# Kernel optimization log

Hardware: AMD Instinct MI355X
Metric: run time of the kernel (lower is better)

Reference implementation:

```python
import jax, jax.numpy as jnp
import numpy as np

N_EMBD = 1024
N_HEAD = 16
B, T = 2, 2048
LN_EPS = 1e-5


def _linear_params(key, d_in, d_out):
    k1, k2 = jax.random.split(key)
    bound = 1.0 / np.sqrt(d_in)
    W = jax.random.uniform(k1, (d_in, d_out), jnp.float32, -bound, bound)
    b = jax.random.uniform(k2, (d_out,), jnp.float32, -bound, bound)
    return W, b


def setup_inputs() -> dict:
    key = jax.random.key(0)
    ks = jax.random.split(key, 8)
    x = jax.random.normal(ks[0], (B, T, N_EMBD), jnp.float32)
    Wq, bq = _linear_params(ks[1], N_EMBD, N_EMBD)
    Wk, bk = _linear_params(ks[2], N_EMBD, N_EMBD)
    Wv, bv = _linear_params(ks[3], N_EMBD, N_EMBD)
    Wo, bo = _linear_params(ks[4], N_EMBD, N_EMBD)
    W1, b1 = _linear_params(ks[5], N_EMBD, 4 * N_EMBD)
    W2, b2 = _linear_params(ks[6], 4 * N_EMBD, N_EMBD)
    ln1_g = jnp.ones((N_EMBD,), jnp.float32)
    ln1_b = jnp.zeros((N_EMBD,), jnp.float32)
    ln2_g = jnp.ones((N_EMBD,), jnp.float32)
    ln2_b = jnp.zeros((N_EMBD,), jnp.float32)
    return dict(x=x, Wq=Wq, bq=bq, Wk=Wk, bk=bk, Wv=Wv, bv=bv, Wo=Wo, bo=bo,
                W1=W1, b1=b1, W2=W2, b2=b2,
                ln1_g=ln1_g, ln1_b=ln1_b, ln2_g=ln2_g, ln2_b=ln2_b)


def _layernorm(x, g, b):
    mu = jnp.mean(x, axis=-1, keepdims=True)
    var = jnp.mean(jnp.square(x - mu), axis=-1, keepdims=True)
    return (x - mu) * jax.lax.rsqrt(var + LN_EPS) * g + b


def _attention(x, Wq, bq, Wk, bk, Wv, bv, Wo, bo):
    Bsz, Tlen, C = x.shape
    hd = C // N_HEAD
    q = (x @ Wq + bq).reshape(Bsz, Tlen, N_HEAD, hd)
    k = (x @ Wk + bk).reshape(Bsz, Tlen, N_HEAD, hd)
    v = (x @ Wv + bv).reshape(Bsz, Tlen, N_HEAD, hd)
    scale = 1.0 / np.sqrt(hd)
    # NOTE: the original module's mask buffer is all ones -> masked_fill is a
    # no-op, so attention is FULL (non-causal) despite the class name.
    att = jnp.einsum('bqhd,bkhd->bhqk', q, k) * scale
    att = jax.nn.softmax(att, axis=-1)
    y = jnp.einsum('bhqk,bkhd->bqhd', att, v).reshape(Bsz, Tlen, C)
    return y @ Wo + bo


def reference(x, Wq, bq, Wk, bk, Wv, bv, Wo, bo, W1, b1, W2, b2,
              ln1_g, ln1_b, ln2_g, ln2_b):
    x = x + _attention(_layernorm(x, ln1_g, ln1_b), Wq, bq, Wk, bk, Wv, bv, Wo, bo)
    h = _layernorm(x, ln2_g, ln2_b)
    h = jax.nn.gelu(h @ W1 + b1, approximate=False) @ W2 + b2
    return x + h
```

## Files before the change

### kernel.cpp

```cpp
#include <hip/hip_runtime.h>
#include <hip/hip_bf16.h>
#include <math.h>


typedef __bf16 bf16x8 __attribute__((ext_vector_type(8)));
typedef float f32x4 __attribute__((ext_vector_type(4)));

__device__ __forceinline__ unsigned short f2bf(float f) {
  union { float f; unsigned int u; } v; v.f = f;
  unsigned int u = v.u;
  unsigned int r = (u + 0x7fffu + ((u >> 16) & 1u)) >> 16;
  return (unsigned short)r;
}

__device__ __forceinline__ unsigned int fbits(float f) {
  union { float f; unsigned int u; } v; v.f = f;
  return v.u;
}

__device__ __forceinline__ bf16x8 ld_bf16x8(const unsigned short* p) {
  union { uint4 u; bf16x8 v; } x;
  x.u = *(const uint4*)p;
  return x.v;
}

__device__ __forceinline__ void async_copy16(const void* g, void* l) {
  __builtin_amdgcn_global_load_lds(
      (const __attribute__((address_space(1))) void*)g,
      (__attribute__((address_space(3))) void*)l, 16, 0, 0);
}

__global__ __launch_bounds__(256) void transpose_cast_kernel(
    const float* __restrict__ W, unsigned short* __restrict__ Wt, int N, int K) {
  __shared__ unsigned short tile[32][33];
  const int n0 = blockIdx.x * 32, k0 = blockIdx.y * 32;
  const int t = threadIdx.x;
  const int r = t >> 3, cq = (t & 7) * 4;
  float4 v = *(const float4*)&W[(size_t)(k0 + r) * N + n0 + cq];
  tile[cq + 0][r] = f2bf(v.x);
  tile[cq + 1][r] = f2bf(v.y);
  tile[cq + 2][r] = f2bf(v.z);
  tile[cq + 3][r] = f2bf(v.w);
  __syncthreads();
  ushort4 o;
  o.x = tile[r][cq + 0];
  o.y = tile[r][cq + 1];
  o.z = tile[r][cq + 2];
  o.w = tile[r][cq + 3];
  *(ushort4*)&Wt[(size_t)(n0 + r) * K + k0 + cq] = o;
}

__global__ __launch_bounds__(256) void transpose_v_kernel(
    const unsigned short* __restrict__ V, unsigned short* __restrict__ Vt) {
  __shared__ unsigned short tile[32][36];
  const int kt = blockIdx.x * 32;
  const int d0 = blockIdx.y * 32;
  const int bh = blockIdx.z;
  const int bb = bh >> 4, h = bh & 15;
  const int t = threadIdx.x;
  const int r = t >> 3, c4 = (t & 7) * 4;
  ushort4 v = *(const ushort4*)&V[((size_t)bb * 2048 + kt + r) * 1024 + h * 64 + d0 + c4];
  tile[c4 + 0][r] = v.x;
  tile[c4 + 1][r] = v.y;
  tile[c4 + 2][r] = v.z;
  tile[c4 + 3][r] = v.w;
  __syncthreads();
  ushort4 o;
  o.x = tile[r][c4 + 0];
  o.y = tile[r][c4 + 1];
  o.z = tile[r][c4 + 2];
  o.w = tile[r][c4 + 3];
  *(ushort4*)&Vt[((size_t)bh * 64 + d0 + r) * 2048 + kt + c4] = o;
}

__global__ __launch_bounds__(256) void ln_kernel(
    const float* __restrict__ x, const float* __restrict__ g,
    const float* __restrict__ b, unsigned short* __restrict__ out) {
  const int row = blockIdx.x, t = threadIdx.x;
  const float4 v = ((const float4*)(x + (size_t)row * 1024))[t];
  float s = v.x + v.y + v.z + v.w;
  float s2 = v.x * v.x + v.y * v.y + v.z * v.z + v.w * v.w;
  for (int o = 32; o > 0; o >>= 1) {
    s += __shfl_xor(s, o, 64);
    s2 += __shfl_xor(s2, o, 64);
  }
  __shared__ float red[8];
  const int w = t >> 6;
  if ((t & 63) == 0) { red[w] = s; red[4 + w] = s2; }
  __syncthreads();
  s = red[0] + red[1] + red[2] + red[3];
  s2 = red[4] + red[5] + red[6] + red[7];
  const float mu = s * (1.f / 1024.f);
  const float var = s2 * (1.f / 1024.f) - mu * mu;
  const float rs = rsqrtf(var + 1e-5f);
  const float4 gg = ((const float4*)g)[t];
  const float4 bb = ((const float4*)b)[t];
  ushort4 o4;
  o4.x = f2bf((v.x - mu) * rs * gg.x + bb.x);
  o4.y = f2bf((v.y - mu) * rs * gg.y + bb.y);
  o4.z = f2bf((v.z - mu) * rs * gg.z + bb.z);
  o4.w = f2bf((v.w - mu) * rs * gg.w + bb.w);
  ((ushort4*)(out + (size_t)row * 1024))[t] = o4;
}

enum { MODE_QKV = 0, MODE_RES = 1, MODE_GELU = 2 };

#define QSCALE 0.18033688011112043f

template <int BM, int BN, int MODE>
__global__ __launch_bounds__(256) void gemm_kernel(
    const unsigned short* __restrict__ A, const unsigned short* __restrict__ Bt,
    const float* __restrict__ bias0, const float* __restrict__ bias1,
    const float* __restrict__ bias2, const float* __restrict__ residual,
    void* __restrict__ out0, void* __restrict__ out1, void* __restrict__ out2,
    int M, int N, int K) {
  constexpr int MI = BM / 32;
  constexpr int NI = BN / 32;
  __shared__ __align__(16) unsigned short As[2][BM * 32];
  __shared__ __align__(16) unsigned short Bs[2][BN * 32];
  const int t = threadIdx.x;
  const int m0 = blockIdx.y * BM, n0 = blockIdx.x * BN;
  const int l = t & 63, w = t >> 6;
  const int wm = (w >> 1) * (BM / 2), wn = (w & 1) * (BN / 2);
  const int lr = l & 15, lq = l >> 4;

  f32x4 acc[MI][NI];
#pragma unroll
  for (int i = 0; i < MI; i++)
#pragma unroll
    for (int j = 0; j < NI; j++) {
      f32x4 z = {0.f, 0.f, 0.f, 0.f};
      acc[i][j] = z;
    }

  for (int k0 = 0; k0 < K; k0 += 64) {
    __syncthreads();
#pragma unroll
    for (int h = 0; h < 2; h++)
#pragma unroll
      for (int s = 0; s < BM / 64; s++) {
        const int c = t + s * 256;
        const int row = c >> 2, k8 = (c & 3) * 8;
        async_copy16(&A[(size_t)(m0 + row) * K + k0 + h * 32 + k8],
                     &As[h][c * 8]);
      }
#pragma unroll
    for (int h = 0; h < 2; h++)
#pragma unroll
      for (int s = 0; s < BN / 64; s++) {
        const int c = t + s * 256;
        const int row = c >> 2, k8 = (c & 3) * 8;
        async_copy16(&Bt[(size_t)(n0 + row) * K + k0 + h * 32 + k8],
                     &Bs[h][c * 8]);
      }
    __syncthreads();
#pragma unroll
    for (int kk = 0; kk < 2; kk++) {
      bf16x8 af[MI], bf[NI];
#pragma unroll
      for (int mi = 0; mi < MI; mi++)
        af[mi] = ld_bf16x8(&As[kk][(wm + mi * 16 + lr) * 32 + lq * 8]);
#pragma unroll
      for (int ni = 0; ni < NI; ni++)
        bf[ni] = ld_bf16x8(&Bs[kk][(wn + ni * 16 + lr) * 32 + lq * 8]);
#pragma unroll
      for (int mi = 0; mi < MI; mi++)
#pragma unroll
        for (int ni = 0; ni < NI; ni++)
          acc[mi][ni] = __builtin_amdgcn_mfma_f32_16x16x32_bf16(
              af[mi], bf[ni], acc[mi][ni], 0, 0, 0);
    }
  }

#pragma unroll
  for (int mi = 0; mi < MI; mi++) {
#pragma unroll
    for (int ni = 0; ni < NI; ni++) {
#pragma unroll
      for (int i = 0; i < 4; i++) {
        const int gm = m0 + wm + mi * 16 + lq * 4 + i;
        const int gn = n0 + wn + ni * 16 + lr;
        const float v = acc[mi][ni][i];
        if (MODE == MODE_QKV) {
          const int sel = gn >> 10, cn = gn & 1023;
          const float* bb = sel == 0 ? bias0 : (sel == 1 ? bias1 : bias2);
          unsigned short* dst =
              (unsigned short*)(sel == 0 ? out0 : (sel == 1 ? out1 : out2));
          float u = v + bb[cn];
          if (sel == 0) u *= QSCALE;
          dst[(size_t)gm * 1024 + cn] = f2bf(u);
        } else if (MODE == MODE_RES) {
          ((float*)out0)[(size_t)gm * N + gn] =
              v + bias0[gn] + residual[(size_t)gm * N + gn];
        } else {
          const float u = v + bias0[gn];
          const float ge = 0.5f * u * (1.f + erff(u * 0.70710678118654752f));
          ((unsigned short*)out0)[(size_t)gm * N + gn] = f2bf(ge);
        }
      }
    }
  }
}

__global__ __launch_bounds__(256) void attn_kernel(
    const unsigned short* __restrict__ Q, const unsigned short* __restrict__ Kt,
    const unsigned short* __restrict__ Vt, unsigned short* __restrict__ O) {
  __shared__ __align__(16) unsigned short QPs[128 * 72];
  __shared__ __align__(16) unsigned short Ks[64 * 72];
  __shared__ __align__(16) unsigned short Vs[64 * 72];
  const int qt = blockIdx.x;
  const int bh = blockIdx.y;
  const int bb = bh >> 4, h = bh & 15;
  const int t = threadIdx.x, l = t & 63, w = t >> 6;
  const int lr = l & 15, lq = l >> 4;
  const size_t rowBase = (size_t)bb * 2048;
  const int col0 = h * 64;

#pragma unroll
  for (int s = 0; s < 4; s++) {
    const int c = t + s * 256;
    const int r = c >> 3, c8 = (c & 7) * 8;
    *(uint4*)&QPs[r * 72 + c8] =
        *(const uint4*)&Q[(rowBase + qt * 128 + r) * 1024 + col0 + c8];
  }
  __syncthreads();
  bf16x8 qf[2][2];
#pragma unroll
  for (int s = 0; s < 2; s++)
#pragma unroll
    for (int kk = 0; kk < 2; kk++)
      qf[s][kk] = ld_bf16x8(&QPs[(w * 32 + s * 16 + lr) * 72 + kk * 32 + lq * 8]);

  f32x4 oacc[2][4];
#pragma unroll
  for (int s = 0; s < 2; s++)
#pragma unroll
    for (int nt = 0; nt < 4; nt++) {
      f32x4 z = {0.f, 0.f, 0.f, 0.f};
      oacc[s][nt] = z;
    }
  float mi_[2] = {-1e30f, -1e30f};
  float lp[2] = {0.f, 0.f};

  for (int kt = 0; kt < 2048; kt += 64) {
    __syncthreads();
#pragma unroll
    for (int s = 0; s < 2; s++) {
      const int c = t + s * 256;
      const int r = c >> 3, c8 = (c & 7) * 8;
      *(uint4*)&Ks[r * 72 + c8] =
          *(const uint4*)&Kt[(rowBase + kt + r) * 1024 + col0 + c8];
      *(uint4*)&Vs[r * 72 + c8] =
          *(const uint4*)&Vt[((size_t)bh * 64 + r) * 2048 + kt + c8];
    }
    __syncthreads();

    f32x4 st[2][4];
#pragma unroll
    for (int s = 0; s < 2; s++)
#pragma unroll
      for (int nt = 0; nt < 4; nt++) {
        f32x4 z = {0.f, 0.f, 0.f, 0.f};
        st[s][nt] = z;
      }
#pragma unroll
    for (int nt = 0; nt < 4; nt++)
#pragma unroll
      for (int kk = 0; kk < 2; kk++) {
        bf16x8 kf = ld_bf16x8(&Ks[(nt * 16 + lr) * 72 + kk * 32 + lq * 8]);
        st[0][nt] = __builtin_amdgcn_mfma_f32_16x16x32_bf16(kf, qf[0][kk], st[0][nt], 0, 0, 0);
        st[1][nt] = __builtin_amdgcn_mfma_f32_16x16x32_bf16(kf, qf[1][kk], st[1][nt], 0, 0, 0);
      }

#pragma unroll
    for (int s = 0; s < 2; s++) {
      float mx = st[s][0][0];
#pragma unroll
      for (int nt = 0; nt < 4; nt++)
#pragma unroll
        for (int i = 0; i < 4; i++) mx = fmaxf(mx, st[s][nt][i]);
      mx = fmaxf(mx, __shfl_xor(mx, 16, 64));
      mx = fmaxf(mx, __shfl_xor(mx, 32, 64));
      const float mnew = fmaxf(mi_[s], mx);
      const float alpha = exp2f(mi_[s] - mnew);
      mi_[s] = mnew;
      float rsum = 0.f;
#pragma unroll
      for (int nt = 0; nt < 4; nt++)
#pragma unroll
        for (int i = 0; i < 4; i++) {
          const float p = exp2f(st[s][nt][i] - mnew);
          st[s][nt][i] = p;
          rsum += p;
        }
      lp[s] = lp[s] * alpha + rsum;
#pragma unroll
      for (int nt = 0; nt < 4; nt++) oacc[s][nt] *= alpha;
    }

#pragma unroll
    for (int s = 0; s < 2; s++)
#pragma unroll
      for (int nt = 0; nt < 4; nt++) {
        uint2 pk;
        pk.x = __builtin_amdgcn_perm(fbits(st[s][nt][1]), fbits(st[s][nt][0]), 0x07060302u);
        pk.y = __builtin_amdgcn_perm(fbits(st[s][nt][3]), fbits(st[s][nt][2]), 0x07060302u);
        *(uint2*)&QPs[(w * 32 + s * 16 + lr) * 72 + nt * 16 + lq * 4] = pk;
      }

#pragma unroll
    for (int kb = 0; kb < 2; kb++) {
      bf16x8 pf0 = ld_bf16x8(&QPs[(w * 32 + lr) * 72 + kb * 32 + lq * 8]);
      bf16x8 pf1 = ld_bf16x8(&QPs[(w * 32 + 16 + lr) * 72 + kb * 32 + lq * 8]);
#pragma unroll
      for (int nt = 0; nt < 4; nt++) {
        bf16x8 vf = ld_bf16x8(&Vs[(nt * 16 + lr) * 72 + kb * 32 + lq * 8]);
        oacc[0][nt] = __builtin_amdgcn_mfma_f32_16x16x32_bf16(pf0, vf, oacc[0][nt], 0, 0, 0);
        oacc[1][nt] = __builtin_amdgcn_mfma_f32_16x16x32_bf16(pf1, vf, oacc[1][nt], 0, 0, 0);
      }
    }
  }

#pragma unroll
  for (int s = 0; s < 2; s++) {
    float li = lp[s];
    li += __shfl_xor(li, 16, 64);
    li += __shfl_xor(li, 32, 64);
    const float inv = 1.f / li;
#pragma unroll
    for (int nt = 0; nt < 4; nt++)
#pragma unroll
      for (int i = 0; i < 4; i++) {
        const size_t orow = rowBase + qt * 128 + w * 32 + s * 16 + lq * 4 + i;
        const int ocol = col0 + nt * 16 + lr;
        O[orow * 1024 + ocol] = f2bf(oacc[s][nt][i] * inv);
      }
  }
}

extern "C" void kernel_launch(void* const* d_in, const int* in_sizes, int n_in,
                              void* d_out, int out_size, void* d_ws, size_t ws_size,
                              hipStream_t stream) {
  const float* x    = (const float*)d_in[0];
  const float* Wq   = (const float*)d_in[1];
  const float* bq   = (const float*)d_in[2];
  const float* Wk   = (const float*)d_in[3];
  const float* bk   = (const float*)d_in[4];
  const float* Wv   = (const float*)d_in[5];
  const float* bv   = (const float*)d_in[6];
  const float* Wo   = (const float*)d_in[7];
  const float* bo   = (const float*)d_in[8];
  const float* W1   = (const float*)d_in[9];
  const float* b1   = (const float*)d_in[10];
  const float* W2   = (const float*)d_in[11];
  const float* b2   = (const float*)d_in[12];
  const float* ln1g = (const float*)d_in[13];
  const float* ln1b = (const float*)d_in[14];
  const float* ln2g = (const float*)d_in[15];
  const float* ln2b = (const float*)d_in[16];

  char* ws = (char*)d_ws;
  const size_t MB = 1024ull * 1024ull;
  unsigned short* WqT = (unsigned short*)(ws + 0 * MB);
  unsigned short* WkT = (unsigned short*)(ws + 2 * MB);
  unsigned short* WvT = (unsigned short*)(ws + 4 * MB);
  unsigned short* WoT = (unsigned short*)(ws + 6 * MB);
  unsigned short* W1T = (unsigned short*)(ws + 8 * MB);
  unsigned short* W2T = (unsigned short*)(ws + 16 * MB);
  unsigned short* xn  = (unsigned short*)(ws + 24 * MB);
  unsigned short* Qb  = (unsigned short*)(ws + 32 * MB);
  unsigned short* Kb  = (unsigned short*)(ws + 40 * MB);
  unsigned short* Vb  = (unsigned short*)(ws + 48 * MB);
  unsigned short* Ob  = (unsigned short*)(ws + 56 * MB);
  float*          x1  = (float*)(ws + 64 * MB);
  unsigned short* h2  = (unsigned short*)(ws + 80 * MB);
  unsigned short* VtG = (unsigned short*)(ws + 24 * MB);
  unsigned short* Hb  = (unsigned short*)(ws + 24 * MB);

  const dim3 blk(256);

  transpose_cast_kernel<<<dim3(32, 32), blk, 0, stream>>>(Wq, WqT, 1024, 1024);
  transpose_cast_kernel<<<dim3(32, 32), blk, 0, stream>>>(Wk, WkT, 1024, 1024);
  transpose_cast_kernel<<<dim3(32, 32), blk, 0, stream>>>(Wv, WvT, 1024, 1024);
  transpose_cast_kernel<<<dim3(32, 32), blk, 0, stream>>>(Wo, WoT, 1024, 1024);
  transpose_cast_kernel<<<dim3(128, 32), blk, 0, stream>>>(W1, W1T, 4096, 1024);
  transpose_cast_kernel<<<dim3(32, 128), blk, 0, stream>>>(W2, W2T, 1024, 4096);

  ln_kernel<<<4096, blk, 0, stream>>>(x, ln1g, ln1b, xn);

  gemm_kernel<128, 128, MODE_QKV><<<dim3(24, 32), blk, 0, stream>>>(
      xn, WqT, bq, bk, bv, nullptr, Qb, Kb, Vb, 4096, 3072, 1024);

  transpose_v_kernel<<<dim3(64, 2, 32), blk, 0, stream>>>(Vb, VtG);

  attn_kernel<<<dim3(16, 32), blk, 0, stream>>>(Qb, Kb, VtG, Ob);

  gemm_kernel<64, 128, MODE_RES><<<dim3(8, 64), blk, 0, stream>>>(
      Ob, WoT, bo, nullptr, nullptr, x, x1, nullptr, nullptr, 4096, 1024, 1024);

  ln_kernel<<<4096, blk, 0, stream>>>(x1, ln2g, ln2b, h2);

  gemm_kernel<128, 128, MODE_GELU><<<dim3(32, 32), blk, 0, stream>>>(
      h2, W1T, b1, nullptr, nullptr, nullptr, Hb, nullptr, nullptr, 4096, 4096, 1024);

  gemm_kernel<64, 128, MODE_RES><<<dim3(8, 64), blk, 0, stream>>>(
      Hb, W2T, b2, nullptr, nullptr, x1, (float*)d_out, nullptr, nullptr, 4096, 1024, 4096);
}
```

Before: 425.5 us.

## Remap GEMM blocks per XCD and halve attention query tile to 64 rows

GEMM launches become 1D grids whose block IDs are remapped so that each of the eight XCDs (blocks assigned round-robin) handles a contiguous band of M tiles, improving L2 reuse of A rows within an XCD. The attention kernel now processes 64 query rows per block (16 per wave) instead of 128, doubling the grid to raise occupancy and parallelism on the many-CU device. The trade-off is that each block reloads the full K and V for half as many queries, doubling K/V traffic, with less MFMA work per LDS load.

```diff
diff --git a/kernel.cpp b/kernel.cpp
--- a/kernel.cpp
+++ b/kernel.cpp
@@ -119,7 +119,14 @@
   __shared__ __align__(16) unsigned short As[2][BM * 32];
   __shared__ __align__(16) unsigned short Bs[2][BN * 32];
   const int t = threadIdx.x;
-  const int m0 = blockIdx.y * BM, n0 = blockIdx.x * BN;
+
+  const int NT = N / BN, MT = M / BM;
+  const int bid = blockIdx.x;
+  const int xcd = bid & 7, local = bid >> 3;
+  const int mt = xcd * (MT >> 3) + local / NT;
+  const int nt_ = local % NT;
+  const int m0 = mt * BM, n0 = nt_ * BN;
+
   const int l = t & 63, w = t >> 6;
   const int wm = (w >> 1) * (BM / 2), wn = (w & 1) * (BN / 2);
   const int lr = l & 15, lq = l >> 4;
@@ -205,7 +212,7 @@
 __global__ __launch_bounds__(256) void attn_kernel(
     const unsigned short* __restrict__ Q, const unsigned short* __restrict__ Kt,
     const unsigned short* __restrict__ Vt, unsigned short* __restrict__ O) {
-  __shared__ __align__(16) unsigned short QPs[128 * 72];
+  __shared__ __align__(16) unsigned short QPs[64 * 72];
   __shared__ __align__(16) unsigned short Ks[64 * 72];
   __shared__ __align__(16) unsigned short Vs[64 * 72];
   const int qt = blockIdx.x;
@@ -217,30 +224,26 @@
   const int col0 = h * 64;
 
 #pragma unroll
-  for (int s = 0; s < 4; s++) {
+  for (int s = 0; s < 2; s++) {
     const int c = t + s * 256;
     const int r = c >> 3, c8 = (c & 7) * 8;
     *(uint4*)&QPs[r * 72 + c8] =
-        *(const uint4*)&Q[(rowBase + qt * 128 + r) * 1024 + col0 + c8];
+        *(const uint4*)&Q[(rowBase + qt * 64 + r) * 1024 + col0 + c8];
   }
   __syncthreads();
-  bf16x8 qf[2][2];
-#pragma unroll
-  for (int s = 0; s < 2; s++)
-#pragma unroll
-    for (int kk = 0; kk < 2; kk++)
-      qf[s][kk] = ld_bf16x8(&QPs[(w * 32 + s * 16 + lr) * 72 + kk * 32 + lq * 8]);
-
-  f32x4 oacc[2][4];
-#pragma unroll
-  for (int s = 0; s < 2; s++)
-#pragma unroll
-    for (int nt = 0; nt < 4; nt++) {
-      f32x4 z = {0.f, 0.f, 0.f, 0.f};
-      oacc[s][nt] = z;
-    }
-  float mi_[2] = {-1e30f, -1e30f};
-  float lp[2] = {0.f, 0.f};
+  bf16x8 qf[2];
+#pragma unroll
+  for (int kk = 0; kk < 2; kk++)
+    qf[kk] = ld_bf16x8(&QPs[(w * 16 + lr) * 72 + kk * 32 + lq * 8]);
+
+  f32x4 oacc[4];
+#pragma unroll
+  for (int nt = 0; nt < 4; nt++) {
+    f32x4 z = {0.f, 0.f, 0.f, 0.f};
+    oacc[nt] = z;
+  }
+  float mi_ = -1e30f;
+  float lp = 0.f;
 
   for (int kt = 0; kt < 2048; kt += 64) {
     __syncthreads();
@@ -255,87 +258,74 @@
     }
     __syncthreads();
 
-    f32x4 st[2][4];
-#pragma unroll
-    for (int s = 0; s < 2; s++)
-#pragma unroll
-      for (int nt = 0; nt < 4; nt++) {
-        f32x4 z = {0.f, 0.f, 0.f, 0.f};
-        st[s][nt] = z;
-      }
+    f32x4 st[4];
+#pragma unroll
+    for (int nt = 0; nt < 4; nt++) {
+      f32x4 z = {0.f, 0.f, 0.f, 0.f};
+      st[nt] = z;
+    }
 #pragma unroll
     for (int nt = 0; nt < 4; nt++)
 #pragma unroll
       for (int kk = 0; kk < 2; kk++) {
         bf16x8 kf = ld_bf16x8(&Ks[(nt * 16 + lr) * 72 + kk * 32 + lq * 8]);
-        st[0][nt] = __builtin_amdgcn_mfma_f32_16x16x32_bf16(kf, qf[0][kk], st[0][nt], 0, 0, 0);
-        st[1][nt] = __builtin_amdgcn_mfma_f32_16x16x32_bf16(kf, qf[1][kk], st[1][nt], 0, 0, 0);
-      }
-
-#pragma unroll
-    for (int s = 0; s < 2; s++) {
-      float mx = st[s][0][0];
-#pragma unroll
-      for (int nt = 0; nt < 4; nt++)
-#pragma unroll
-        for (int i = 0; i < 4; i++) mx = fmaxf(mx, st[s][nt][i]);
-      mx = fmaxf(mx, __shfl_xor(mx, 16, 64));
-      mx = fmaxf(mx, __shfl_xor(mx, 32, 64));
-      const float mnew = fmaxf(mi_[s], mx);
-      const float alpha = exp2f(mi_[s] - mnew);
-      mi_[s] = mnew;
-      float rsum = 0.f;
-#pragma unroll
-      for (int nt = 0; nt < 4; nt++)
-#pragma unroll
-        for (int i = 0; i < 4; i++) {
-          const float p = exp2f(st[s][nt][i] - mnew);
-          st[s][nt][i] = p;
-          rsum += p;
-        }
-      lp[s] = lp[s] * alpha + rsum;
-#pragma unroll
-      for (int nt = 0; nt < 4; nt++) oacc[s][nt] *= alpha;
-    }
-
-#pragma unroll
-    for (int s = 0; s < 2; s++)
-#pragma unroll
-      for (int nt = 0; nt < 4; nt++) {
-        uint2 pk;
-        pk.x = __builtin_amdgcn_perm(fbits(st[s][nt][1]), fbits(st[s][nt][0]), 0x07060302u);
-        pk.y = __builtin_amdgcn_perm(fbits(st[s][nt][3]), fbits(st[s][nt][2]), 0x07060302u);
-        *(uint2*)&QPs[(w * 32 + s * 16 + lr) * 72 + nt * 16 + lq * 4] = pk;
-      }
+        st[nt] = __builtin_amdgcn_mfma_f32_16x16x32_bf16(kf, qf[kk], st[nt], 0, 0, 0);
+      }
+
+    float mx = st[0][0];
+#pragma unroll
+    for (int nt = 0; nt < 4; nt++)
+#pragma unroll
+      for (int i = 0; i < 4; i++) mx = fmaxf(mx, st[nt][i]);
+    mx = fmaxf(mx, __shfl_xor(mx, 16, 64));
+    mx = fmaxf(mx, __shfl_xor(mx, 32, 64));
+    const float mnew = fmaxf(mi_, mx);
+    const float alpha = exp2f(mi_ - mnew);
+    mi_ = mnew;
+    float rsum = 0.f;
+#pragma unroll
+    for (int nt = 0; nt < 4; nt++)
+#pragma unroll
+      for (int i = 0; i < 4; i++) {
+        const float p = exp2f(st[nt][i] - mnew);
+        st[nt][i] = p;
+        rsum += p;
+      }
+    lp = lp * alpha + rsum;
+#pragma unroll
+    for (int nt = 0; nt < 4; nt++) oacc[nt] *= alpha;
+
+#pragma unroll
+    for (int nt = 0; nt < 4; nt++) {
+      uint2 pk;
+      pk.x = __builtin_amdgcn_perm(fbits(st[nt][1]), fbits(st[nt][0]), 0x07060302u);
+      pk.y = __builtin_amdgcn_perm(fbits(st[nt][3]), fbits(st[nt][2]), 0x07060302u);
+      *(uint2*)&QPs[(w * 16 + lr) * 72 + nt * 16 + lq * 4] = pk;
+    }
 
 #pragma unroll
     for (int kb = 0; kb < 2; kb++) {
-      bf16x8 pf0 = ld_bf16x8(&QPs[(w * 32 + lr) * 72 + kb * 32 + lq * 8]);
-      bf16x8 pf1 = ld_bf16x8(&QPs[(w * 32 + 16 + lr) * 72 + kb * 32 + lq * 8]);
+      bf16x8 pf = ld_bf16x8(&QPs[(w * 16 + lr) * 72 + kb * 32 + lq * 8]);
 #pragma unroll
       for (int nt = 0; nt < 4; nt++) {
         bf16x8 vf = ld_bf16x8(&Vs[(nt * 16 + lr) * 72 + kb * 32 + lq * 8]);
-        oacc[0][nt] = __builtin_amdgcn_mfma_f32_16x16x32_bf16(pf0, vf, oacc[0][nt], 0, 0, 0);
-        oacc[1][nt] = __builtin_amdgcn_mfma_f32_16x16x32_bf16(pf1, vf, oacc[1][nt], 0, 0, 0);
-      }
-    }
-  }
-
-#pragma unroll
-  for (int s = 0; s < 2; s++) {
-    float li = lp[s];
-    li += __shfl_xor(li, 16, 64);
-    li += __shfl_xor(li, 32, 64);
-    const float inv = 1.f / li;
-#pragma unroll
-    for (int nt = 0; nt < 4; nt++)
-#pragma unroll
-      for (int i = 0; i < 4; i++) {
-        const size_t orow = rowBase + qt * 128 + w * 32 + s * 16 + lq * 4 + i;
-        const int ocol = col0 + nt * 16 + lr;
-        O[orow * 1024 + ocol] = f2bf(oacc[s][nt][i] * inv);
-      }
-  }
+        oacc[nt] = __builtin_amdgcn_mfma_f32_16x16x32_bf16(pf, vf, oacc[nt], 0, 0, 0);
+      }
+    }
+  }
+
+  float li = lp;
+  li += __shfl_xor(li, 16, 64);
+  li += __shfl_xor(li, 32, 64);
+  const float inv = 1.f / li;
+#pragma unroll
+  for (int nt = 0; nt < 4; nt++)
+#pragma unroll
+    for (int i = 0; i < 4; i++) {
+      const size_t orow = rowBase + qt * 64 + w * 16 + lq * 4 + i;
+      const int ocol = col0 + nt * 16 + lr;
+      O[orow * 1024 + ocol] = f2bf(oacc[nt][i] * inv);
+    }
 }
 
 extern "C" void kernel_launch(void* const* d_in, const int* in_sizes, int n_in,
@@ -388,21 +378,21 @@
 
   ln_kernel<<<4096, blk, 0, stream>>>(x, ln1g, ln1b, xn);
 
-  gemm_kernel<128, 128, MODE_QKV><<<dim3(24, 32), blk, 0, stream>>>(
+  gemm_kernel<128, 128, MODE_QKV><<<dim3(24 * 32), blk, 0, stream>>>(
       xn, WqT, bq, bk, bv, nullptr, Qb, Kb, Vb, 4096, 3072, 1024);
 
   transpose_v_kernel<<<dim3(64, 2, 32), blk, 0, stream>>>(Vb, VtG);
 
-  attn_kernel<<<dim3(16, 32), blk, 0, stream>>>(Qb, Kb, VtG, Ob);
-
-  gemm_kernel<64, 128, MODE_RES><<<dim3(8, 64), blk, 0, stream>>>(
+  attn_kernel<<<dim3(32, 32), blk, 0, stream>>>(Qb, Kb, VtG, Ob);
+
+  gemm_kernel<64, 128, MODE_RES><<<dim3(8 * 64), blk, 0, stream>>>(
       Ob, WoT, bo, nullptr, nullptr, x, x1, nullptr, nullptr, 4096, 1024, 1024);
 
   ln_kernel<<<4096, blk, 0, stream>>>(x1, ln2g, ln2b, h2);
 
-  gemm_kernel<128, 128, MODE_GELU><<<dim3(32, 32), blk, 0, stream>>>(
+  gemm_kernel<128, 128, MODE_GELU><<<dim3(32 * 32), blk, 0, stream>>>(
       h2, W1T, b1, nullptr, nullptr, nullptr, Hb, nullptr, nullptr, 4096, 4096, 1024);
 
-  gemm_kernel<64, 128, MODE_RES><<<dim3(8, 64), blk, 0, stream>>>(
+  gemm_kernel<64, 128, MODE_RES><<<dim3(8 * 64), blk, 0, stream>>>(
       Hb, W2T, b2, nullptr, nullptr, x1, (float*)d_out, nullptr, nullptr, 4096, 1024, 4096);
 }
```

After: 424.7 us. Within noise of the previous version (-0.2%).

## Double-buffer GEMM loads, remap blocks per XCD, and widen attention KV tiles

Applied to the files above, without the earlier changes.

The GEMM kernel now double-buffers its shared-memory tiles, so the async copies for the next K slice are issued before computing on the current one, and it uses one barrier per iteration instead of two. Blocks are launched on a 1D grid and remapped so that each of the 8 XCDs gets a contiguous band of M tiles, which is meant to improve L2 reuse. The attention kernel processes 128 keys per iteration instead of 64, halving the number of barriers and softmax rescale steps at the cost of more shared memory and registers. The GEMM's shared memory doubles, which may lower occupancy. Reusing the single-barrier buffer depends on the async copies completing correctly before the data is read.

```diff
diff --git a/kernel.cpp b/kernel.cpp
--- a/kernel.cpp
+++ b/kernel.cpp
@@ -116,10 +116,17 @@
     int M, int N, int K) {
   constexpr int MI = BM / 32;
   constexpr int NI = BN / 32;
-  __shared__ __align__(16) unsigned short As[2][BM * 32];
-  __shared__ __align__(16) unsigned short Bs[2][BN * 32];
+  __shared__ __align__(16) unsigned short As[2][2][BM * 32];
+  __shared__ __align__(16) unsigned short Bs[2][2][BN * 32];
   const int t = threadIdx.x;
-  const int m0 = blockIdx.y * BM, n0 = blockIdx.x * BN;
+
+  const int NT = N / BN, MT = M / BM;
+  const int bid = blockIdx.x;
+  const int xcd = bid & 7, local = bid >> 3;
+  const int mt = xcd * (MT >> 3) + local / NT;
+  const int nt_ = local % NT;
+  const int m0 = mt * BM, n0 = nt_ * BN;
+
   const int l = t & 63, w = t >> 6;
   const int wm = (w >> 1) * (BM / 2), wn = (w & 1) * (BN / 2);
   const int lr = l & 15, lq = l >> 4;
@@ -133,8 +140,7 @@
       acc[i][j] = z;
     }
 
-  for (int k0 = 0; k0 < K; k0 += 64) {
-    __syncthreads();
+  auto issue = [&](int k0, int p) {
 #pragma unroll
     for (int h = 0; h < 2; h++)
 #pragma unroll
@@ -142,7 +148,7 @@
         const int c = t + s * 256;
         const int row = c >> 2, k8 = (c & 3) * 8;
         async_copy16(&A[(size_t)(m0 + row) * K + k0 + h * 32 + k8],
-                     &As[h][c * 8]);
+                     &As[p][h][c * 8]);
       }
 #pragma unroll
     for (int h = 0; h < 2; h++)
@@ -151,18 +157,24 @@
         const int c = t + s * 256;
         const int row = c >> 2, k8 = (c & 3) * 8;
         async_copy16(&Bt[(size_t)(n0 + row) * K + k0 + h * 32 + k8],
-                     &Bs[h][c * 8]);
-      }
+                     &Bs[p][h][c * 8]);
+      }
+  };
+
+  issue(0, 0);
+  int p = 0;
+  for (int k0 = 0; k0 < K; k0 += 64) {
     __syncthreads();
+    if (k0 + 64 < K) issue(k0 + 64, p ^ 1);
 #pragma unroll
     for (int kk = 0; kk < 2; kk++) {
       bf16x8 af[MI], bf[NI];
 #pragma unroll
       for (int mi = 0; mi < MI; mi++)
-        af[mi] = ld_bf16x8(&As[kk][(wm + mi * 16 + lr) * 32 + lq * 8]);
+        af[mi] = ld_bf16x8(&As[p][kk][(wm + mi * 16 + lr) * 32 + lq * 8]);
 #pragma unroll
       for (int ni = 0; ni < NI; ni++)
-        bf[ni] = ld_bf16x8(&Bs[kk][(wn + ni * 16 + lr) * 32 + lq * 8]);
+        bf[ni] = ld_bf16x8(&Bs[p][kk][(wn + ni * 16 + lr) * 32 + lq * 8]);
 #pragma unroll
       for (int mi = 0; mi < MI; mi++)
 #pragma unroll
@@ -170,6 +182,7 @@
           acc[mi][ni] = __builtin_amdgcn_mfma_f32_16x16x32_bf16(
               af[mi], bf[ni], acc[mi][ni], 0, 0, 0);
     }
+    p ^= 1;
   }
 
 #pragma unroll
@@ -206,8 +219,8 @@
     const unsigned short* __restrict__ Q, const unsigned short* __restrict__ Kt,
     const unsigned short* __restrict__ Vt, unsigned short* __restrict__ O) {
   __shared__ __align__(16) unsigned short QPs[128 * 72];
-  __shared__ __align__(16) unsigned short Ks[64 * 72];
-  __shared__ __align__(16) unsigned short Vs[64 * 72];
+  __shared__ __align__(16) unsigned short Ks[128 * 72];
+  __shared__ __align__(16) unsigned short Vs[64 * 136];
   const int qt = blockIdx.x;
   const int bh = blockIdx.y;
   const int bb = bh >> 4, h = bh & 15;
@@ -242,29 +255,30 @@
   float mi_[2] = {-1e30f, -1e30f};
   float lp[2] = {0.f, 0.f};
 
-  for (int kt = 0; kt < 2048; kt += 64) {
+  for (int kt = 0; kt < 2048; kt += 128) {
     __syncthreads();
 #pragma unroll
-    for (int s = 0; s < 2; s++) {
+    for (int s = 0; s < 4; s++) {
       const int c = t + s * 256;
       const int r = c >> 3, c8 = (c & 7) * 8;
       *(uint4*)&Ks[r * 72 + c8] =
           *(const uint4*)&Kt[(rowBase + kt + r) * 1024 + col0 + c8];
-      *(uint4*)&Vs[r * 72 + c8] =
-          *(const uint4*)&Vt[((size_t)bh * 64 + r) * 2048 + kt + c8];
+      const int vr = c >> 4, vc = (c & 15) * 8;
+      *(uint4*)&Vs[vr * 136 + vc] =
+          *(const uint4*)&Vt[((size_t)bh * 64 + vr) * 2048 + kt + vc];
     }
     __syncthreads();
 
-    f32x4 st[2][4];
+    f32x4 st[2][8];
 #pragma unroll
     for (int s = 0; s < 2; s++)
 #pragma unroll
-      for (int nt = 0; nt < 4; nt++) {
+      for (int nt = 0; nt < 8; nt++) {
         f32x4 z = {0.f, 0.f, 0.f, 0.f};
         st[s][nt] = z;
       }
 #pragma unroll
-    for (int nt = 0; nt < 4; nt++)
+    for (int nt = 0; nt < 8; nt++)
 #pragma unroll
       for (int kk = 0; kk < 2; kk++) {
         bf16x8 kf = ld_bf16x8(&Ks[(nt * 16 + lr) * 72 + kk * 32 + lq * 8]);
@@ -276,7 +290,7 @@
     for (int s = 0; s < 2; s++) {
       float mx = st[s][0][0];
 #pragma unroll
-      for (int nt = 0; nt < 4; nt++)
+      for (int nt = 0; nt < 8; nt++)
 #pragma unroll
         for (int i = 0; i < 4; i++) mx = fmaxf(mx, st[s][nt][i]);
       mx = fmaxf(mx, __shfl_xor(mx, 16, 64));
@@ -286,7 +300,7 @@
       mi_[s] = mnew;
       float rsum = 0.f;
 #pragma unroll
-      for (int nt = 0; nt < 4; nt++)
+      for (int nt = 0; nt < 8; nt++)
 #pragma unroll
         for (int i = 0; i < 4; i++) {
           const float p = exp2f(st[s][nt][i] - mnew);
@@ -299,24 +313,27 @@
     }
 
 #pragma unroll
-    for (int s = 0; s < 2; s++)
-#pragma unroll
-      for (int nt = 0; nt < 4; nt++) {
-        uint2 pk;
-        pk.x = __builtin_amdgcn_perm(fbits(st[s][nt][1]), fbits(st[s][nt][0]), 0x07060302u);
-        pk.y = __builtin_amdgcn_perm(fbits(st[s][nt][3]), fbits(st[s][nt][2]), 0x07060302u);
-        *(uint2*)&QPs[(w * 32 + s * 16 + lr) * 72 + nt * 16 + lq * 4] = pk;
-      }
-
-#pragma unroll
-    for (int kb = 0; kb < 2; kb++) {
-      bf16x8 pf0 = ld_bf16x8(&QPs[(w * 32 + lr) * 72 + kb * 32 + lq * 8]);
-      bf16x8 pf1 = ld_bf16x8(&QPs[(w * 32 + 16 + lr) * 72 + kb * 32 + lq * 8]);
-#pragma unroll
-      for (int nt = 0; nt < 4; nt++) {
-        bf16x8 vf = ld_bf16x8(&Vs[(nt * 16 + lr) * 72 + kb * 32 + lq * 8]);
-        oacc[0][nt] = __builtin_amdgcn_mfma_f32_16x16x32_bf16(pf0, vf, oacc[0][nt], 0, 0, 0);
-        oacc[1][nt] = __builtin_amdgcn_mfma_f32_16x16x32_bf16(pf1, vf, oacc[1][nt], 0, 0, 0);
+    for (int hh = 0; hh < 2; hh++) {
+#pragma unroll
+      for (int s = 0; s < 2; s++)
+#pragma unroll
+        for (int n4 = 0; n4 < 4; n4++) {
+          const int nt = hh * 4 + n4;
+          uint2 pk;
+          pk.x = __builtin_amdgcn_perm(fbits(st[s][nt][1]), fbits(st[s][nt][0]), 0x07060302u);
+          pk.y = __builtin_amdgcn_perm(fbits(st[s][nt][3]), fbits(st[s][nt][2]), 0x07060302u);
+          *(uint2*)&QPs[(w * 32 + s * 16 + lr) * 72 + n4 * 16 + lq * 4] = pk;
+        }
+#pragma unroll
+      for (int kb = 0; kb < 2; kb++) {
+        bf16x8 pf0 = ld_bf16x8(&QPs[(w * 32 + lr) * 72 + kb * 32 + lq * 8]);
+        bf16x8 pf1 = ld_bf16x8(&QPs[(w * 32 + 16 + lr) * 72 + kb * 32 + lq * 8]);
+#pragma unroll
+        for (int n4 = 0; n4 < 4; n4++) {
+          bf16x8 vf = ld_bf16x8(&Vs[(n4 * 16 + lr) * 136 + hh * 64 + kb * 32 + lq * 8]);
+          oacc[0][n4] = __builtin_amdgcn_mfma_f32_16x16x32_bf16(pf0, vf, oacc[0][n4], 0, 0, 0);
+          oacc[1][n4] = __builtin_amdgcn_mfma_f32_16x16x32_bf16(pf1, vf, oacc[1][n4], 0, 0, 0);
+        }
       }
     }
   }
@@ -388,21 +405,21 @@
 
   ln_kernel<<<4096, blk, 0, stream>>>(x, ln1g, ln1b, xn);
 
-  gemm_kernel<128, 128, MODE_QKV><<<dim3(24, 32), blk, 0, stream>>>(
+  gemm_kernel<128, 128, MODE_QKV><<<dim3(24 * 32), blk, 0, stream>>>(
       xn, WqT, bq, bk, bv, nullptr, Qb, Kb, Vb, 4096, 3072, 1024);
 
   transpose_v_kernel<<<dim3(64, 2, 32), blk, 0, stream>>>(Vb, VtG);
 
   attn_kernel<<<dim3(16, 32), blk, 0, stream>>>(Qb, Kb, VtG, Ob);
 
-  gemm_kernel<64, 128, MODE_RES><<<dim3(8, 64), blk, 0, stream>>>(
+  gemm_kernel<64, 128, MODE_RES><<<dim3(8 * 64), blk, 0, stream>>>(
       Ob, WoT, bo, nullptr, nullptr, x, x1, nullptr, nullptr, 4096, 1024, 1024);
 
   ln_kernel<<<4096, blk, 0, stream>>>(x1, ln2g, ln2b, h2);
 
-  gemm_kernel<128, 128, MODE_GELU><<<dim3(32, 32), blk, 0, stream>>>(
+  gemm_kernel<128, 128, MODE_GELU><<<dim3(32 * 32), blk, 0, stream>>>(
       h2, W1T, b1, nullptr, nullptr, nullptr, Hb, nullptr, nullptr, 4096, 4096, 1024);
 
-  gemm_kernel<64, 128, MODE_RES><<<dim3(8, 64), blk, 0, stream>>>(
+  gemm_kernel<64, 128, MODE_RES><<<dim3(8 * 64), blk, 0, stream>>>(
       Hb, W2T, b2, nullptr, nullptr, x1, (float*)d_out, nullptr, nullptr, 4096, 1024, 4096);
 }
```

After: 424.4 us. No clear change (-0.3%).
